# Optimization experiments

Hardware: AMD Instinct MI355X
Metric: run time of the kernel (lower is better)

The kernel has to match this reference:

```python
import jax, jax.numpy as jnp
import numpy as np

NEG_SLOPE = 0.2  # PyG GATConv default negative_slope


def gat_layer(x, src, dst, W, a_src, a_dst, bias, concat, N):
    """PyG GATConv: h = xW; e_ij = LeakyReLU(a_src.h_j + a_dst.h_i);
    alpha = segment-softmax over incoming edges of i; out_i = sum_j alpha_ij h_j."""
    H, C = a_src.shape
    h = (x @ W).reshape(N, H, C)                      # [N,H,C]
    alpha_s = jnp.einsum('nhc,hc->nh', h, a_src)      # [N,H]
    alpha_d = jnp.einsum('nhc,hc->nh', h, a_dst)      # [N,H]
    e = jax.nn.leaky_relu(alpha_s[src] + alpha_d[dst], NEG_SLOPE)  # [E,H]
    # numerically-stable segment softmax over destination nodes
    m = jax.ops.segment_max(e, dst, num_segments=N)   # [N,H]
    e = jnp.exp(e - m[dst])
    denom = jax.ops.segment_sum(e, dst, num_segments=N)
    alpha = e / (denom[dst] + 1e-16)                  # [E,H]
    msg = h[src] * alpha[:, :, None]                  # [E,H,C]
    out = jax.ops.segment_sum(msg, dst, num_segments=N)  # [N,H,C]
    out = out.reshape(N, H * C) if concat else out.mean(axis=1)
    return out + bias


def setup_inputs() -> dict:
    key = jax.random.key(0)
    ks = jax.random.split(key, 12)
    N, E, F_IN, C, H = 50000, 800000, 512, 32, 8
    s = 0.05
    x = jax.random.normal(ks[0], (N, F_IN), dtype=jnp.float32)
    edge_index = jax.random.randint(ks[1], (2, E), 0, N, dtype=jnp.int64)
    W1 = jax.random.normal(ks[2], (F_IN, H * C), dtype=jnp.float32) * s
    as1 = jax.random.normal(ks[3], (H, C), dtype=jnp.float32) * s
    ad1 = jax.random.normal(ks[4], (H, C), dtype=jnp.float32) * s
    b1 = jnp.zeros((H * C,), dtype=jnp.float32)
    W2 = jax.random.normal(ks[5], (H * C, H * C), dtype=jnp.float32) * s
    as2 = jax.random.normal(ks[6], (H, C), dtype=jnp.float32) * s
    ad2 = jax.random.normal(ks[7], (H, C), dtype=jnp.float32) * s
    b2 = jnp.zeros((C,), dtype=jnp.float32)
    Wp = jax.random.normal(ks[8], (C, 1), dtype=jnp.float32) * s
    bp = jnp.zeros((1,), dtype=jnp.float32)
    return {"edge_index": edge_index, "x": x, "W1": W1, "as1": as1, "ad1": ad1,
            "b1": b1, "W2": W2, "as2": as2, "ad2": ad2, "b2": b2,
            "Wp": Wp, "bp": bp}


def reference(edge_index, x, W1, as1, ad1, b1, W2, as2, ad2, b2, Wp, bp):
    N = x.shape[0]
    # PyG GATConv adds self-loops by default
    loops = jnp.arange(N, dtype=edge_index.dtype)
    src = jnp.concatenate([edge_index[0], loops])
    dst = jnp.concatenate([edge_index[1], loops])
    h = gat_layer(x, src, dst, W1, as1, ad1, b1, concat=True, N=N)
    h = jax.nn.relu(h)
    # F.dropout(training=self.training) is identity in eval mode
    h = gat_layer(h, src, dst, W2, as2, ad2, b2, concat=False, N=N)
    return jax.nn.sigmoid(h @ Wp + bp)   # [N,1]
```

## Files before the change

kernel.cpp:

```cpp
#include <hip/hip_runtime.h>
#include <math.h>

#define H_HEADS 8
#define C_DIM   32
#define HC      256
#define F_IN    512
#define NEG_SLOPE 0.2f

typedef __attribute__((ext_vector_type(8))) short    bf16x8;
typedef __attribute__((ext_vector_type(4))) short    s16x4;
typedef __attribute__((ext_vector_type(4))) float    f32x4;
typedef __attribute__((ext_vector_type(2))) float    f32x2;
typedef __attribute__((ext_vector_type(8))) _Float16 h16x8;

__device__ __forceinline__ short f2bf(float f) {
    union { float f; unsigned u; } v; v.f = f;
    unsigned r = v.u + 0x7FFF + ((v.u >> 16) & 1);
    return (short)(r >> 16);
}

__device__ __forceinline__ void gl2lds16(const short* g, short* l) {
    __builtin_amdgcn_global_load_lds(
        (const __attribute__((address_space(1))) void*)g,
        (__attribute__((address_space(3))) void*)l, 16, 0, 0);
}

__global__ void wfrag_kernel(const float* __restrict__ W, short* __restrict__ Wf, int K)
{
    int tid = blockIdx.x * 256 + threadIdx.x;
    if (tid >= K * HC) return;
    int j  = tid & 7;
    int l  = (tid >> 3) & 63;
    int nb = (tid >> 9) & 15;
    int s  = tid >> 13;
    int k  = s * 32 + (l >> 4) * 8 + j;
    int n  = nb * 16 + (l & 15);
    Wf[tid] = f2bf(W[(size_t)k * HC + n]);
}

template<bool ABF16>
__global__ __launch_bounds__(256) void gemm_mfma(const void* __restrict__ Aptr,
    const short* __restrict__ Bf, unsigned char* __restrict__ h8,
    const float* __restrict__ a_s, const float* __restrict__ a_d,
    float* __restrict__ alpha_s, float* __restrict__ alpha_d, int M, int K)
{
    __shared__ short Bs[2][8192];
    __shared__ float Als[512], Ald[512];

    const int tid  = threadIdx.x;
    const int w    = tid >> 6;
    const int lane = tid & 63;
    const int quad = lane >> 4;
    const int ml   = lane & 15;
    const int bm   = blockIdx.x * 64;

    const int rowA = bm + w * 16 + ml;
    const int rowL = rowA < M ? rowA : M - 1;

    f32x4 acc[16];
    #pragma unroll
    for (int nb = 0; nb < 16; ++nb) acc[nb] = (f32x4){0.f, 0.f, 0.f, 0.f};

    const float* A32 = (const float*)Aptr;
    const short* A16 = (const short*)Aptr;
    const int nsteps = K >> 5;

    {
        const short* g = Bf + (size_t)w * 2048 + lane * 8;
        short* l = &Bs[0][w * 2048];
        #pragma unroll
        for (int c = 0; c < 4; ++c) gl2lds16(g + c * 512, l + c * 512);
    }

    float4 p0, p1;
    bf16x8 pb;
    if (ABF16) {
        pb = *(const bf16x8*)(A16 + (size_t)rowL * K + quad * 8);
    } else {
        const float* ap = A32 + (size_t)rowL * K + quad * 8;
        p0 = *(const float4*)(ap);
        p1 = *(const float4*)(ap + 4);
    }

    for (int s = 0; s < nsteps; ++s) {
        __syncthreads();

        if (s + 1 < nsteps) {
            const short* g = Bf + (size_t)(s + 1) * 8192 + w * 2048 + lane * 8;
            short* l = &Bs[(s + 1) & 1][w * 2048];
            #pragma unroll
            for (int c = 0; c < 4; ++c) gl2lds16(g + c * 512, l + c * 512);
        }

        bf16x8 af;
        if (ABF16) {
            af = pb;
            if (s + 1 < nsteps)
                pb = *(const bf16x8*)(A16 + (size_t)rowL * K + (s + 1) * 32 + quad * 8);
        } else {
            af[0] = f2bf(p0.x); af[1] = f2bf(p0.y); af[2] = f2bf(p0.z); af[3] = f2bf(p0.w);
            af[4] = f2bf(p1.x); af[5] = f2bf(p1.y); af[6] = f2bf(p1.z); af[7] = f2bf(p1.w);
            if (s + 1 < nsteps) {
                const float* ap = A32 + (size_t)rowL * K + (s + 1) * 32 + quad * 8;
                p0 = *(const float4*)(ap);
                p1 = *(const float4*)(ap + 4);
            }
        }

        const short* bsrc = &Bs[s & 1][lane * 8];
        #pragma unroll
        for (int nb = 0; nb < 16; ++nb) {
            bf16x8 bfr = *(const bf16x8*)(bsrc + nb * 512);
            acc[nb] = __builtin_amdgcn_mfma_f32_16x16x32_bf16(af, bfr, acc[nb], 0, 0, 0);
        }
    }

    float as_v[16], ad_v[16];
    #pragma unroll
    for (int nb = 0; nb < 16; ++nb) {
        as_v[nb] = a_s[nb * 16 + ml];
        ad_v[nb] = a_d[nb * 16 + ml];
    }

    #pragma unroll
    for (int r = 0; r < 4; ++r) {
        const int rl  = w * 16 + quad * 4 + r;
        const int row = bm + rl;

        if (row < M) {
            unsigned char* hrow = h8 + (size_t)row * HC;
            #pragma unroll
            for (int i = 0; i < 8; ++i) {
                int pk = __builtin_amdgcn_cvt_pk_fp8_f32(acc[2 * i][r], acc[2 * i + 1][r], 0, false);
                hrow[(2 * i) * 16 + ml]     = (unsigned char)(pk & 0xFF);
                hrow[(2 * i + 1) * 16 + ml] = (unsigned char)((pk >> 8) & 0xFF);
            }
        }

        float hs[8], hd[8];
        #pragma unroll
        for (int q = 0; q < 8; ++q) {
            hs[q] = acc[2 * q][r] * as_v[2 * q] + acc[2 * q + 1][r] * as_v[2 * q + 1];
            hd[q] = acc[2 * q][r] * ad_v[2 * q] + acc[2 * q + 1][r] * ad_v[2 * q + 1];
        }
        #pragma unroll
        for (int off = 1; off < 16; off <<= 1) {
            #pragma unroll
            for (int q = 0; q < 8; ++q) {
                hs[q] += __shfl_xor(hs[q], off);
                hd[q] += __shfl_xor(hd[q], off);
            }
        }
        if (ml == 0) {
            #pragma unroll
            for (int q = 0; q < 8; ++q) {
                Als[rl * 8 + q] = hs[q];
                Ald[rl * 8 + q] = hd[q];
            }
        }
    }
    __syncthreads();
    #pragma unroll
    for (int k = 0; k < 2; ++k) {
        int idx = tid + k * 256;
        int rl = idx >> 3, q = idx & 7;
        int row = bm + rl;
        if (row < M) {
            alpha_s[(size_t)row * H_HEADS + q] = Als[idx];
            alpha_d[(size_t)row * H_HEADS + q] = Ald[idx];
        }
    }
}

__global__ __launch_bounds__(256) void wcalc_kernel(const int2* __restrict__ es,
    const float* __restrict__ alpha_s, const float* __restrict__ alpha_d,
    _Float16* __restrict__ wq, int P)
{
    int p = blockIdx.x * 256 + threadIdx.x;
    if (p >= P) return;
    int2 sd = es[p];
    const float4* as = (const float4*)(alpha_s + (size_t)sd.x * H_HEADS);
    const float4* ad = (const float4*)(alpha_d + (size_t)sd.y * H_HEADS);
    float4 s0 = as[0], s1 = as[1], d0 = ad[0], d1 = ad[1];
    float e[8] = {s0.x + d0.x, s0.y + d0.y, s0.z + d0.z, s0.w + d0.w,
                  s1.x + d1.x, s1.y + d1.y, s1.z + d1.z, s1.w + d1.w};
    h16x8 o;
    #pragma unroll
    for (int h = 0; h < 8; ++h) {
        float v = e[h] > 0.f ? e[h] : NEG_SLOPE * e[h];
        o[h] = (_Float16)__expf(v);
    }
    *(h16x8*)(wq + (size_t)p * H_HEADS) = o;
}

__global__ void zero_int(int* __restrict__ p, int n)
{
    int i = blockIdx.x * 256 + threadIdx.x;
    if (i < n) p[i] = 0;
}

__global__ void hist_kernel(const int* __restrict__ ei, int E, int N,
                            int* __restrict__ cnt)
{
    int e = blockIdx.x * 256 + threadIdx.x;
    if (e < E) atomicAdd(&cnt[ei[E + e]], 1);
    else if (e < E + N) atomicAdd(&cnt[e - E], 1);
}

__global__ __launch_bounds__(256) void scan_sum(const int* __restrict__ cnt, int n,
                                                int* __restrict__ chunk_sum)
{
    __shared__ int lds[256];
    int b = blockIdx.x, t = threadIdx.x;
    int base = b * 1024 + t * 4;
    int s = 0;
    #pragma unroll
    for (int j = 0; j < 4; ++j) { int i = base + j; if (i < n) s += cnt[i]; }
    lds[t] = s; __syncthreads();
    for (int off = 128; off > 0; off >>= 1) {
        if (t < off) lds[t] += lds[t + off];
        __syncthreads();
    }
    if (t == 0) chunk_sum[b] = lds[0];
}

__global__ void scan_top(const int* __restrict__ chunk_sum, int nch,
                         int* __restrict__ chunk_off, int* __restrict__ row_ptr,
                         int n_nodes)
{
    int t = threadIdx.x;
    int v = (t < nch) ? chunk_sum[t] : 0;
    int inc = v;
    #pragma unroll
    for (int off = 1; off < 64; off <<= 1) {
        int u = __shfl_up(inc, off);
        if (t >= off) inc += u;
    }
    if (t < nch) chunk_off[t] = inc - v;
    if (t == 63) row_ptr[n_nodes] = inc;
}

__global__ __launch_bounds__(256) void scan_local(const int* __restrict__ cnt, int n,
    const int* __restrict__ chunk_off, int* __restrict__ row_ptr)
{
    __shared__ int lds[256];
    int b = blockIdx.x, t = threadIdx.x;
    int base = b * 1024 + t * 4;
    int v[4]; int s = 0;
    #pragma unroll
    for (int j = 0; j < 4; ++j) { int i = base + j; v[j] = (i < n) ? cnt[i] : 0; s += v[j]; }
    lds[t] = s; __syncthreads();
    for (int off = 1; off < 256; off <<= 1) {
        int u = (t >= off) ? lds[t - off] : 0;
        __syncthreads();
        lds[t] += u;
        __syncthreads();
    }
    int run = lds[t] - s + chunk_off[b];
    #pragma unroll
    for (int j = 0; j < 4; ++j) {
        int i = base + j;
        if (i < n) row_ptr[i] = run;
        run += v[j];
    }
}

__global__ void scatter_kernel(const int* __restrict__ ei, int E, int N,
    const int* __restrict__ row_ptr, int* __restrict__ fill, int2* __restrict__ es)
{
    int e = blockIdx.x * 256 + threadIdx.x;
    int src, dst;
    if (e < E)          { src = ei[e]; dst = ei[E + e]; }
    else if (e < E + N) { src = dst = e - E; }
    else return;
    int pos = row_ptr[dst] + atomicAdd(&fill[dst], 1);
    es[pos] = make_int2(src, dst);
}

__global__ __launch_bounds__(256) void agg1_kernel(const unsigned* __restrict__ h8,
    const _Float16* __restrict__ wq, const int* __restrict__ row_ptr,
    const int2* __restrict__ es, const float* __restrict__ bias,
    short* __restrict__ z_bf, int N)
{
    const int l = threadIdx.x & 63;
    const int i = blockIdx.x * 4 + (threadIdx.x >> 6);
    if (i >= N) return;
    const int hh = l >> 3;
    const int beg = row_ptr[i], end = row_ptr[i + 1];
    f32x4 acc = {0.f, 0.f, 0.f, 0.f};
    float dsum = 0.f;
    int p = beg;
    for (; p + 7 < end; p += 8) {
        int s[8]; float w[8]; unsigned hv[8];
        #pragma unroll
        for (int u = 0; u < 8; ++u) s[u] = es[p + u].x;
        #pragma unroll
        for (int u = 0; u < 8; ++u) w[u] = (float)wq[(size_t)(p + u) * 8 + hh];
        #pragma unroll
        for (int u = 0; u < 8; ++u) hv[u] = h8[(size_t)s[u] * 64 + l];
        #pragma unroll
        for (int u = 0; u < 8; ++u) {
            f32x2 lo = __builtin_amdgcn_cvt_pk_f32_fp8(hv[u], false);
            f32x2 hi = __builtin_amdgcn_cvt_pk_f32_fp8(hv[u], true);
            acc[0] = fmaf(w[u], lo[0], acc[0]);
            acc[1] = fmaf(w[u], lo[1], acc[1]);
            acc[2] = fmaf(w[u], hi[0], acc[2]);
            acc[3] = fmaf(w[u], hi[1], acc[3]);
            dsum += w[u];
        }
    }
    for (; p < end; ++p) {
        int s0 = es[p].x;
        float w0 = (float)wq[(size_t)p * 8 + hh];
        unsigned hv = h8[(size_t)s0 * 64 + l];
        f32x2 lo = __builtin_amdgcn_cvt_pk_f32_fp8(hv, false);
        f32x2 hi = __builtin_amdgcn_cvt_pk_f32_fp8(hv, true);
        acc[0] = fmaf(w0, lo[0], acc[0]);
        acc[1] = fmaf(w0, lo[1], acc[1]);
        acc[2] = fmaf(w0, hi[0], acc[2]);
        acc[3] = fmaf(w0, hi[1], acc[3]);
        dsum += w0;
    }
    float inv = 1.f / (dsum + 1e-16f);
    s16x4 pk;
    #pragma unroll
    for (int j = 0; j < 4; ++j) {
        float z = acc[j] * inv + bias[4 * l + j];
        pk[j] = f2bf(z > 0.f ? z : 0.f);
    }
    *(s16x4*)(z_bf + (size_t)i * HC + 4 * l) = pk;
}

__global__ __launch_bounds__(256) void agg2_kernel(const unsigned* __restrict__ h8,
    const _Float16* __restrict__ wq, const int* __restrict__ row_ptr,
    const int2* __restrict__ es, const float* __restrict__ b2,
    const float* __restrict__ Wp, const float* __restrict__ bp,
    float* __restrict__ out, int N)
{
    const int l = threadIdx.x & 63;
    const int i = blockIdx.x * 4 + (threadIdx.x >> 6);
    if (i >= N) return;
    const int hh = l >> 3;
    const int beg = row_ptr[i], end = row_ptr[i + 1];
    f32x4 acc = {0.f, 0.f, 0.f, 0.f};
    float dsum = 0.f;
    int p = beg;
    for (; p + 7 < end; p += 8) {
        int s[8]; float w[8]; unsigned hv[8];
        #pragma unroll
        for (int u = 0; u < 8; ++u) s[u] = es[p + u].x;
        #pragma unroll
        for (int u = 0; u < 8; ++u) w[u] = (float)wq[(size_t)(p + u) * 8 + hh];
        #pragma unroll
        for (int u = 0; u < 8; ++u) hv[u] = h8[(size_t)s[u] * 64 + l];
        #pragma unroll
        for (int u = 0; u < 8; ++u) {
            f32x2 lo = __builtin_amdgcn_cvt_pk_f32_fp8(hv[u], false);
            f32x2 hi = __builtin_amdgcn_cvt_pk_f32_fp8(hv[u], true);
            acc[0] = fmaf(w[u], lo[0], acc[0]);
            acc[1] = fmaf(w[u], lo[1], acc[1]);
            acc[2] = fmaf(w[u], hi[0], acc[2]);
            acc[3] = fmaf(w[u], hi[1], acc[3]);
            dsum += w[u];
        }
    }
    for (; p < end; ++p) {
        int s0 = es[p].x;
        float w0 = (float)wq[(size_t)p * 8 + hh];
        unsigned hv = h8[(size_t)s0 * 64 + l];
        f32x2 lo = __builtin_amdgcn_cvt_pk_f32_fp8(hv, false);
        f32x2 hi = __builtin_amdgcn_cvt_pk_f32_fp8(hv, true);
        acc[0] = fmaf(w0, lo[0], acc[0]);
        acc[1] = fmaf(w0, lo[1], acc[1]);
        acc[2] = fmaf(w0, hi[0], acc[2]);
        acc[3] = fmaf(w0, hi[1], acc[3]);
        dsum += w0;
    }
    float inv = 1.f / (dsum + 1e-16f);
    int cc = (4 * l) & 31;
    float partial = 0.f;
    #pragma unroll
    for (int j = 0; j < 4; ++j) partial = fmaf(acc[j] * inv, Wp[cc + j], partial);
    if (l < 8) {
        #pragma unroll
        for (int j = 0; j < 4; ++j) partial = fmaf(8.f * b2[4 * l + j], Wp[4 * l + j], partial);
    }
    #pragma unroll
    for (int off = 32; off > 0; off >>= 1) partial += __shfl_xor(partial, off);
    if (l == 0) out[i] = 1.f / (1.f + __expf(-(0.125f * partial + bp[0])));
}

extern "C" void kernel_launch(void* const* d_in, const int* in_sizes, int n_in,
                              void* d_out, int out_size, void* d_ws, size_t ws_size,
                              hipStream_t stream)
{
    const int*   ei  = (const int*)d_in[0];
    const float* x   = (const float*)d_in[1];
    const float* W1  = (const float*)d_in[2];
    const float* as1 = (const float*)d_in[3];
    const float* ad1 = (const float*)d_in[4];
    const float* b1  = (const float*)d_in[5];
    const float* W2  = (const float*)d_in[6];
    const float* as2 = (const float*)d_in[7];
    const float* ad2 = (const float*)d_in[8];
    const float* b2  = (const float*)d_in[9];
    const float* Wp  = (const float*)d_in[10];
    const float* bp  = (const float*)d_in[11];
    float* out = (float*)d_out;

    const int E = in_sizes[0] / 2;
    const int N = in_sizes[1] / F_IN;
    const int ET = E + N;

    float*         asb = (float*)d_ws;
    float*         adb = asb + (size_t)N * H_HEADS;
    unsigned char* h8  = (unsigned char*)(adb + (size_t)N * H_HEADS);
    short*         z1b = (short*)(h8 + (size_t)N * HC);
    short*         Wf1 = z1b + (size_t)N * HC;
    short*         Wf2 = Wf1 + (size_t)F_IN * HC;
    _Float16*      wq  = (_Float16*)(Wf2 + (size_t)HC * HC);
    int2*          es  = (int2*)(wq + (size_t)ET * H_HEADS);
    int* cnt       = (int*)(es + ET);
    int* fill      = cnt + N;
    int* row_ptr   = fill + N;
    int* chunk_off = row_ptr + N + 1;
    int* chunk_sum = chunk_off + 64;

    const int NCH = (N + 1023) / 1024;
    const int MB  = (N + 63) / 64;
    const int NB4 = (N + 3) / 4;

    zero_int<<<(2 * N + 255) / 256, 256, 0, stream>>>(cnt, 2 * N);
    hist_kernel<<<(ET + 255) / 256, 256, 0, stream>>>(ei, E, N, cnt);
    scan_sum<<<NCH, 256, 0, stream>>>(cnt, N, chunk_sum);
    scan_top<<<1, 64, 0, stream>>>(chunk_sum, NCH, chunk_off, row_ptr, N);
    scan_local<<<NCH, 256, 0, stream>>>(cnt, N, chunk_off, row_ptr);
    scatter_kernel<<<(ET + 255) / 256, 256, 0, stream>>>(ei, E, N, row_ptr, fill, es);

    wfrag_kernel<<<(F_IN * HC + 255) / 256, 256, 0, stream>>>(W1, Wf1, F_IN);
    wfrag_kernel<<<(HC * HC + 255) / 256, 256, 0, stream>>>(W2, Wf2, HC);

    gemm_mfma<false><<<MB, 256, 0, stream>>>(x, Wf1, h8, as1, ad1, asb, adb, N, F_IN);
    wcalc_kernel<<<(ET + 255) / 256, 256, 0, stream>>>(es, asb, adb, wq, ET);
    agg1_kernel<<<NB4, 256, 0, stream>>>((const unsigned*)h8, wq, row_ptr, es, b1, z1b, N);

    gemm_mfma<true><<<MB, 256, 0, stream>>>(z1b, Wf2, h8, as2, ad2, asb, adb, N, HC);
    wcalc_kernel<<<(ET + 255) / 256, 256, 0, stream>>>(es, asb, adb, wq, ET);
    agg2_kernel<<<NB4, 256, 0, stream>>>((const unsigned*)h8, wq, row_ptr, es, b2, Wp, bp, out, N);
}
```

Baseline: 423.2 us.

## Split wavefront across four edges with 16-byte gathers in aggregation kernels

Aggregation kernels now assign 16 lanes per edge, each loading 16 fp8 bytes (uint4), so one wavefront processes four edges at once instead of one edge with 4-byte loads per lane. Partial sums are combined with cross-lane shuffles at the end. The scan_top kernel is folded into scan_local via a wave-level reduction over chunk sums, and the scatter reuses the count array with atomicSub, which drops the fill buffer and halves the zeroing. The wider loads cut per-edge memory instructions, at the cost of more registers (16 accumulators) and a shuffle reduction per node.

```diff
diff --git a/kernel.cpp b/kernel.cpp
--- a/kernel.cpp
+++ b/kernel.cpp
@@ -224,27 +224,22 @@
     if (t == 0) chunk_sum[b] = lds[0];
 }
 
-__global__ void scan_top(const int* __restrict__ chunk_sum, int nch,
-                         int* __restrict__ chunk_off, int* __restrict__ row_ptr,
-                         int n_nodes)
-{
-    int t = threadIdx.x;
-    int v = (t < nch) ? chunk_sum[t] : 0;
-    int inc = v;
-    #pragma unroll
-    for (int off = 1; off < 64; off <<= 1) {
-        int u = __shfl_up(inc, off);
-        if (t >= off) inc += u;
-    }
-    if (t < nch) chunk_off[t] = inc - v;
-    if (t == 63) row_ptr[n_nodes] = inc;
-}
-
 __global__ __launch_bounds__(256) void scan_local(const int* __restrict__ cnt, int n,
-    const int* __restrict__ chunk_off, int* __restrict__ row_ptr)
+    const int* __restrict__ chunk_sum, int nch, int* __restrict__ row_ptr)
 {
     __shared__ int lds[256];
     int b = blockIdx.x, t = threadIdx.x;
+    int lane = t & 63;
+
+    int cs  = (lane < nch) ? chunk_sum[lane] : 0;
+    int pre = (lane < b)   ? cs : 0;
+    int tot = cs;
+    #pragma unroll
+    for (int off = 32; off > 0; off >>= 1) {
+        pre += __shfl_xor(pre, off);
+        tot += __shfl_xor(tot, off);
+    }
+
     int base = b * 1024 + t * 4;
     int v[4]; int s = 0;
     #pragma unroll
@@ -256,137 +251,158 @@
         lds[t] += u;
         __syncthreads();
     }
-    int run = lds[t] - s + chunk_off[b];
+    int run = lds[t] - s + pre;
     #pragma unroll
     for (int j = 0; j < 4; ++j) {
         int i = base + j;
         if (i < n) row_ptr[i] = run;
         run += v[j];
     }
+    if (b == gridDim.x - 1 && t == 0) row_ptr[n] = tot;
 }
 
 __global__ void scatter_kernel(const int* __restrict__ ei, int E, int N,
-    const int* __restrict__ row_ptr, int* __restrict__ fill, int2* __restrict__ es)
+    const int* __restrict__ row_ptr, int* __restrict__ cnt, int2* __restrict__ es)
 {
     int e = blockIdx.x * 256 + threadIdx.x;
     int src, dst;
     if (e < E)          { src = ei[e]; dst = ei[E + e]; }
     else if (e < E + N) { src = dst = e - E; }
     else return;
-    int pos = row_ptr[dst] + atomicAdd(&fill[dst], 1);
+    int pos = row_ptr[dst] + atomicSub(&cnt[dst], 1) - 1;
     es[pos] = make_int2(src, dst);
 }
 
-__global__ __launch_bounds__(256) void agg1_kernel(const unsigned* __restrict__ h8,
+#define ACC4(word, wgt, base_) do { \
+    f32x2 lo_ = __builtin_amdgcn_cvt_pk_f32_fp8((word), false); \
+    f32x2 hi_ = __builtin_amdgcn_cvt_pk_f32_fp8((word), true);  \
+    acc[(base_) + 0] = fmaf((wgt), lo_[0], acc[(base_) + 0]); \
+    acc[(base_) + 1] = fmaf((wgt), lo_[1], acc[(base_) + 1]); \
+    acc[(base_) + 2] = fmaf((wgt), hi_[0], acc[(base_) + 2]); \
+    acc[(base_) + 3] = fmaf((wgt), hi_[1], acc[(base_) + 3]); \
+} while (0)
+
+__global__ __launch_bounds__(256) void agg1_kernel(const unsigned char* __restrict__ h8,
     const _Float16* __restrict__ wq, const int* __restrict__ row_ptr,
     const int2* __restrict__ es, const float* __restrict__ bias,
     short* __restrict__ z_bf, int N)
 {
-    const int l = threadIdx.x & 63;
-    const int i = blockIdx.x * 4 + (threadIdx.x >> 6);
+    const int l  = threadIdx.x & 63;
+    const int i  = blockIdx.x * 4 + (threadIdx.x >> 6);
     if (i >= N) return;
-    const int hh = l >> 3;
+    const int c  = l & 15;
+    const int eo = l >> 4;
+    const int hh = c >> 1;
     const int beg = row_ptr[i], end = row_ptr[i + 1];
-    f32x4 acc = {0.f, 0.f, 0.f, 0.f};
+
+    float acc[16];
+    #pragma unroll
+    for (int j = 0; j < 16; ++j) acc[j] = 0.f;
     float dsum = 0.f;
+
     int p = beg;
     for (; p + 7 < end; p += 8) {
-        int s[8]; float w[8]; unsigned hv[8];
-        #pragma unroll
-        for (int u = 0; u < 8; ++u) s[u] = es[p + u].x;
-        #pragma unroll
-        for (int u = 0; u < 8; ++u) w[u] = (float)wq[(size_t)(p + u) * 8 + hh];
-        #pragma unroll
-        for (int u = 0; u < 8; ++u) hv[u] = h8[(size_t)s[u] * 64 + l];
-        #pragma unroll
-        for (int u = 0; u < 8; ++u) {
-            f32x2 lo = __builtin_amdgcn_cvt_pk_f32_fp8(hv[u], false);
-            f32x2 hi = __builtin_amdgcn_cvt_pk_f32_fp8(hv[u], true);
-            acc[0] = fmaf(w[u], lo[0], acc[0]);
-            acc[1] = fmaf(w[u], lo[1], acc[1]);
-            acc[2] = fmaf(w[u], hi[0], acc[2]);
-            acc[3] = fmaf(w[u], hi[1], acc[3]);
-            dsum += w[u];
-        }
-    }
-    for (; p < end; ++p) {
-        int s0 = es[p].x;
-        float w0 = (float)wq[(size_t)p * 8 + hh];
-        unsigned hv = h8[(size_t)s0 * 64 + l];
-        f32x2 lo = __builtin_amdgcn_cvt_pk_f32_fp8(hv, false);
-        f32x2 hi = __builtin_amdgcn_cvt_pk_f32_fp8(hv, true);
-        acc[0] = fmaf(w0, lo[0], acc[0]);
-        acc[1] = fmaf(w0, lo[1], acc[1]);
-        acc[2] = fmaf(w0, hi[0], acc[2]);
-        acc[3] = fmaf(w0, hi[1], acc[3]);
+        int p0 = p + eo, p1 = p + 4 + eo;
+        int s0 = es[p0].x, s1 = es[p1].x;
+        float w0 = (float)wq[(size_t)p0 * 8 + hh];
+        float w1 = (float)wq[(size_t)p1 * 8 + hh];
+        uint4 h0 = *(const uint4*)(h8 + (size_t)s0 * 256 + c * 16);
+        uint4 h1 = *(const uint4*)(h8 + (size_t)s1 * 256 + c * 16);
+        ACC4(h0.x, w0, 0); ACC4(h0.y, w0, 4); ACC4(h0.z, w0, 8); ACC4(h0.w, w0, 12);
+        ACC4(h1.x, w1, 0); ACC4(h1.y, w1, 4); ACC4(h1.z, w1, 8); ACC4(h1.w, w1, 12);
+        dsum += w0 + w1;
+    }
+    for (; p < end; p += 4) {
+        int pe = p + eo;
+        int pc = pe < end ? pe : end - 1;
+        int s0 = es[pc].x;
+        float w0 = pe < end ? (float)wq[(size_t)pc * 8 + hh] : 0.f;
+        uint4 h0 = *(const uint4*)(h8 + (size_t)s0 * 256 + c * 16);
+        ACC4(h0.x, w0, 0); ACC4(h0.y, w0, 4); ACC4(h0.z, w0, 8); ACC4(h0.w, w0, 12);
         dsum += w0;
     }
+
+    #pragma unroll
+    for (int j = 0; j < 16; ++j) {
+        acc[j] += __shfl_xor(acc[j], 32);
+        acc[j] += __shfl_xor(acc[j], 16);
+    }
+    dsum += __shfl_xor(dsum, 32);
+    dsum += __shfl_xor(dsum, 16);
+
     float inv = 1.f / (dsum + 1e-16f);
-    s16x4 pk;
-    #pragma unroll
-    for (int j = 0; j < 4; ++j) {
-        float z = acc[j] * inv + bias[4 * l + j];
-        pk[j] = f2bf(z > 0.f ? z : 0.f);
-    }
-    *(s16x4*)(z_bf + (size_t)i * HC + 4 * l) = pk;
-}
-
-__global__ __launch_bounds__(256) void agg2_kernel(const unsigned* __restrict__ h8,
+    if (eo == 0) {
+        union { short s[16]; bf16x8 v[2]; } zz;
+        #pragma unroll
+        for (int j = 0; j < 16; ++j) {
+            float z = acc[j] * inv + bias[c * 16 + j];
+            zz.s[j] = f2bf(z > 0.f ? z : 0.f);
+        }
+        *(bf16x8*)(z_bf + (size_t)i * HC + c * 16)     = zz.v[0];
+        *(bf16x8*)(z_bf + (size_t)i * HC + c * 16 + 8) = zz.v[1];
+    }
+}
+
+__global__ __launch_bounds__(256) void agg2_kernel(const unsigned char* __restrict__ h8,
     const _Float16* __restrict__ wq, const int* __restrict__ row_ptr,
     const int2* __restrict__ es, const float* __restrict__ b2,
     const float* __restrict__ Wp, const float* __restrict__ bp,
     float* __restrict__ out, int N)
 {
-    const int l = threadIdx.x & 63;
-    const int i = blockIdx.x * 4 + (threadIdx.x >> 6);
+    const int l  = threadIdx.x & 63;
+    const int i  = blockIdx.x * 4 + (threadIdx.x >> 6);
     if (i >= N) return;
-    const int hh = l >> 3;
+    const int c  = l & 15;
+    const int eo = l >> 4;
+    const int hh = c >> 1;
     const int beg = row_ptr[i], end = row_ptr[i + 1];
-    f32x4 acc = {0.f, 0.f, 0.f, 0.f};
+
+    float acc[16];
+    #pragma unroll
+    for (int j = 0; j < 16; ++j) acc[j] = 0.f;
     float dsum = 0.f;
+
     int p = beg;
     for (; p + 7 < end; p += 8) {
-        int s[8]; float w[8]; unsigned hv[8];
-        #pragma unroll
-        for (int u = 0; u < 8; ++u) s[u] = es[p + u].x;
-        #pragma unroll
-        for (int u = 0; u < 8; ++u) w[u] = (float)wq[(size_t)(p + u) * 8 + hh];
-        #pragma unroll
-        for (int u = 0; u < 8; ++u) hv[u] = h8[(size_t)s[u] * 64 + l];
-        #pragma unroll
-        for (int u = 0; u < 8; ++u) {
-            f32x2 lo = __builtin_amdgcn_cvt_pk_f32_fp8(hv[u], false);
-            f32x2 hi = __builtin_amdgcn_cvt_pk_f32_fp8(hv[u], true);
-            acc[0] = fmaf(w[u], lo[0], acc[0]);
-            acc[1] = fmaf(w[u], lo[1], acc[1]);
-            acc[2] = fmaf(w[u], hi[0], acc[2]);
-            acc[3] = fmaf(w[u], hi[1], acc[3]);
-            dsum += w[u];
-        }
-    }
-    for (; p < end; ++p) {
-        int s0 = es[p].x;
-        float w0 = (float)wq[(size_t)p * 8 + hh];
-        unsigned hv = h8[(size_t)s0 * 64 + l];
-        f32x2 lo = __builtin_amdgcn_cvt_pk_f32_fp8(hv, false);
-        f32x2 hi = __builtin_amdgcn_cvt_pk_f32_fp8(hv, true);
-        acc[0] = fmaf(w0, lo[0], acc[0]);
-        acc[1] = fmaf(w0, lo[1], acc[1]);
-        acc[2] = fmaf(w0, hi[0], acc[2]);
-        acc[3] = fmaf(w0, hi[1], acc[3]);
+        int p0 = p + eo, p1 = p + 4 + eo;
+        int s0 = es[p0].x, s1 = es[p1].x;
+        float w0 = (float)wq[(size_t)p0 * 8 + hh];
+        float w1 = (float)wq[(size_t)p1 * 8 + hh];
+        uint4 h0 = *(const uint4*)(h8 + (size_t)s0 * 256 + c * 16);
+        uint4 h1 = *(const uint4*)(h8 + (size_t)s1 * 256 + c * 16);
+        ACC4(h0.x, w0, 0); ACC4(h0.y, w0, 4); ACC4(h0.z, w0, 8); ACC4(h0.w, w0, 12);
+        ACC4(h1.x, w1, 0); ACC4(h1.y, w1, 4); ACC4(h1.z, w1, 8); ACC4(h1.w, w1, 12);
+        dsum += w0 + w1;
+    }
+    for (; p < end; p += 4) {
+        int pe = p + eo;
+        int pc = pe < end ? pe : end - 1;
+        int s0 = es[pc].x;
+        float w0 = pe < end ? (float)wq[(size_t)pc * 8 + hh] : 0.f;
+        uint4 h0 = *(const uint4*)(h8 + (size_t)s0 * 256 + c * 16);
+        ACC4(h0.x, w0, 0); ACC4(h0.y, w0, 4); ACC4(h0.z, w0, 8); ACC4(h0.w, w0, 12);
         dsum += w0;
     }
+
+    #pragma unroll
+    for (int j = 0; j < 16; ++j) {
+        acc[j] += __shfl_xor(acc[j], 32);
+        acc[j] += __shfl_xor(acc[j], 16);
+    }
+    dsum += __shfl_xor(dsum, 32);
+    dsum += __shfl_xor(dsum, 16);
+
     float inv = 1.f / (dsum + 1e-16f);
-    int cc = (4 * l) & 31;
+    const int wb = (c & 1) << 4;
     float partial = 0.f;
     #pragma unroll
-    for (int j = 0; j < 4; ++j) partial = fmaf(acc[j] * inv, Wp[cc + j], partial);
-    if (l < 8) {
-        #pragma unroll
-        for (int j = 0; j < 4; ++j) partial = fmaf(8.f * b2[4 * l + j], Wp[4 * l + j], partial);
-    }
-    #pragma unroll
-    for (int off = 32; off > 0; off >>= 1) partial += __shfl_xor(partial, off);
+    for (int j = 0; j < 16; ++j) partial = fmaf(acc[j] * inv, Wp[wb + j], partial);
+    if (eo == 0 && c < 2) {
+        #pragma unroll
+        for (int j = 0; j < 16; ++j) partial += 8.f * b2[c * 16 + j] * Wp[c * 16 + j];
+    }
+    #pragma unroll
+    for (int off = 8; off > 0; off >>= 1) partial += __shfl_xor(partial, off);
     if (l == 0) out[i] = 1.f / (1.f + __expf(-(0.125f * partial + bp[0])));
 }
 
@@ -421,30 +437,27 @@
     _Float16*      wq  = (_Float16*)(Wf2 + (size_t)HC * HC);
     int2*          es  = (int2*)(wq + (size_t)ET * H_HEADS);
     int* cnt       = (int*)(es + ET);
-    int* fill      = cnt + N;
-    int* row_ptr   = fill + N;
-    int* chunk_off = row_ptr + N + 1;
-    int* chunk_sum = chunk_off + 64;
+    int* row_ptr   = cnt + N;
+    int* chunk_sum = row_ptr + N + 1;
 
     const int NCH = (N + 1023) / 1024;
     const int MB  = (N + 63) / 64;
     const int NB4 = (N + 3) / 4;
 
-    zero_int<<<(2 * N + 255) / 256, 256, 0, stream>>>(cnt, 2 * N);
+    zero_int<<<(N + 255) / 256, 256, 0, stream>>>(cnt, N);
     hist_kernel<<<(ET + 255) / 256, 256, 0, stream>>>(ei, E, N, cnt);
     scan_sum<<<NCH, 256, 0, stream>>>(cnt, N, chunk_sum);
-    scan_top<<<1, 64, 0, stream>>>(chunk_sum, NCH, chunk_off, row_ptr, N);
-    scan_local<<<NCH, 256, 0, stream>>>(cnt, N, chunk_off, row_ptr);
-    scatter_kernel<<<(ET + 255) / 256, 256, 0, stream>>>(ei, E, N, row_ptr, fill, es);
+    scan_local<<<NCH, 256, 0, stream>>>(cnt, N, chunk_sum, NCH, row_ptr);
+    scatter_kernel<<<(ET + 255) / 256, 256, 0, stream>>>(ei, E, N, row_ptr, cnt, es);
 
     wfrag_kernel<<<(F_IN * HC + 255) / 256, 256, 0, stream>>>(W1, Wf1, F_IN);
     wfrag_kernel<<<(HC * HC + 255) / 256, 256, 0, stream>>>(W2, Wf2, HC);
 
     gemm_mfma<false><<<MB, 256, 0, stream>>>(x, Wf1, h8, as1, ad1, asb, adb, N, F_IN);
     wcalc_kernel<<<(ET + 255) / 256, 256, 0, stream>>>(es, asb, adb, wq, ET);
-    agg1_kernel<<<NB4, 256, 0, stream>>>((const unsigned*)h8, wq, row_ptr, es, b1, z1b, N);
+    agg1_kernel<<<NB4, 256, 0, stream>>>(h8, wq, row_ptr, es, b1, z1b, N);
 
     gemm_mfma<true><<<MB, 256, 0, stream>>>(z1b, Wf2, h8, as2, ad2, asb, adb, N, HC);
     wcalc_kernel<<<(ET + 255) / 256, 256, 0, stream>>>(es, asb, adb, wq, ET);
-    agg2_kernel<<<NB4, 256, 0, stream>>>((const unsigned*)h8, wq, row_ptr, es, b2, Wp, bp, out, N);
-}
+    agg2_kernel<<<NB4, 256, 0, stream>>>(h8, wq, row_ptr, es, b2, Wp, bp, out, N);
+}
```

New measurement: 419.9 us. About the same (-0.8%).
